# Kernel tuning notes

Measured on AMD Instinct MI355X. Metric: run time of the kernel, lower is better.

## Reference

```python
import jax, jax.numpy as jnp
import numpy as np
from jax import lax

BN_EPS = 1e-5
DIST_EPS = 1e-8

def _three_nn_interpolate(xyz1, xyz2, points2):
    # squared pairwise distances: (B, N, S)
    d2 = (jnp.sum(xyz1 ** 2, -1)[:, :, None]
          + jnp.sum(xyz2 ** 2, -1)[:, None, :]
          - 2.0 * jnp.einsum('bnd,bsd->bns', xyz1, xyz2))
    neg_d, idx = lax.top_k(-d2, 3)            # 3 nearest -> (B, N, 3)
    dist = -neg_d
    recip = 1.0 / (dist + DIST_EPS)
    weight = recip / jnp.sum(recip, -1, keepdims=True)   # (B, N, 3)
    gathered = jax.vmap(lambda p, i: p[i])(points2, idx)  # (B, N, 3, C2)
    return jnp.einsum('bnkc,bnk->bnc', gathered, weight)

def _conv_bn_relu(x, w, g, b):
    # x: (B, N, Cin); 1x1 conv == matmul; BatchNorm1d over (B, N) per channel (training stats)
    y = jnp.einsum('bnc,oc->bno', x, w)
    mu = jnp.mean(y, axis=(0, 1))
    var = jnp.mean((y - mu) ** 2, axis=(0, 1))
    yn = (y - mu) * lax.rsqrt(var + BN_EPS)
    return jax.nn.relu(yn * g + b)

def setup_inputs() -> dict:
    key = jax.random.key(0)
    ks = jax.random.split(key, 6)
    B, N, S, C1, C2 = 16, 4096, 1024, 256, 256
    return {
        'xyz1': jax.random.normal(ks[0], (B, N, 3), jnp.float32),
        'xyz2': jax.random.normal(ks[1], (B, S, 3), jnp.float32),
        'points1': jax.random.normal(ks[2], (B, N, C1), jnp.float32),
        'points2': jax.random.normal(ks[3], (B, S, C2), jnp.float32),
        'w1': jax.random.normal(ks[4], (256, C1 + C2), jnp.float32) * 0.04,
        'g1': jnp.ones((256,), jnp.float32),
        'b1': jnp.zeros((256,), jnp.float32),
        'w2': jax.random.normal(ks[5], (256, 256), jnp.float32) * 0.06,
        'g2': jnp.ones((256,), jnp.float32),
        'b2': jnp.zeros((256,), jnp.float32),
    }

def reference(xyz1, xyz2, points1, points2, w1, g1, b1, w2, g2, b2):
    interp = _three_nn_interpolate(xyz1, xyz2, points2)    # (B, N, C2)
    feats = jnp.concatenate([points1, interp], axis=-1)    # (B, N, C1+C2)
    h = _conv_bn_relu(feats, w1, g1, b1)
    out = _conv_bn_relu(h, w2, g2, b2)
    return out                                              # (B, N, 256)
```

## Files before the change

### kernel.cpp

```cpp
#include <hip/hip_runtime.h>
#include <stdint.h>

typedef unsigned short ushort_t;
typedef __bf16 bf16x8 __attribute__((ext_vector_type(8)));
typedef float f32x4 __attribute__((ext_vector_type(4)));
typedef unsigned short ushort8 __attribute__((ext_vector_type(8)));
typedef __attribute__((address_space(1))) void GVoid;
typedef __attribute__((address_space(3))) void LVoid;

#define DEV static __device__ __forceinline__

DEV unsigned short f2bf(float f) {
    union { float f; unsigned int i; } v; v.f = f;
    unsigned int u = v.i;
    return (unsigned short)((u + 0x7fffu + ((u >> 16) & 1u)) >> 16);
}
DEV float bf2f(unsigned short u) {
    union { unsigned int i; float f; } v; v.i = ((unsigned int)u) << 16; return v.f;
}

__global__ __launch_bounds__(256) void cvt_kernel(
    const float* __restrict__ in, ushort_t* __restrict__ out, int n)
{
    int i = blockIdx.x * 256 + threadIdx.x;
    if (i < n) out[i] = f2bf(in[i]);
}

__global__ __launch_bounds__(256) void knn_kernel(
    const float* __restrict__ xyz1, const float* __restrict__ xyz2,
    int* __restrict__ idx_out, float* __restrict__ w_out)
{
    __shared__ float4 P[1024];
    __shared__ float mD[12][64];
    __shared__ int   mI[12][64];
    const int b = blockIdx.y;
    const int tid = threadIdx.x;
    for (int s = tid; s < 1024; s += 256) {
        const float* p = xyz2 + ((size_t)b * 1024 + s) * 3;
        float x = p[0], y = p[1], z = p[2];
        float pp = __fadd_rn(__fadd_rn(__fmul_rn(x, x), __fmul_rn(y, y)), __fmul_rn(z, z));
        P[s] = make_float4(x, y, z, pp);
    }
    __syncthreads();
    const int ql = tid & 63;
    const int chunk = tid >> 6;
    const int n = blockIdx.x * 64 + ql;
    const float* q = xyz1 + ((size_t)b * 4096 + n) * 3;
    float qx = q[0], qy = q[1], qz = q[2];
    float qq = __fadd_rn(__fadd_rn(__fmul_rn(qx, qx), __fmul_rn(qy, qy)), __fmul_rn(qz, qz));
    float d0 = 1e30f, d1 = 1e30f, d2 = 1e30f;
    int i0 = 0, i1 = 0, i2 = 0;
    const int s0 = chunk * 256;
#pragma unroll 4
    for (int s = s0; s < s0 + 256; ++s) {
        float4 p = P[s];
        float dot = __fadd_rn(__fadd_rn(__fmul_rn(qx, p.x), __fmul_rn(qy, p.y)), __fmul_rn(qz, p.z));
        float d = __fsub_rn(__fadd_rn(qq, p.w), __fmul_rn(2.0f, dot));
        if (d < d2) {
            if (d < d1) {
                d2 = d1; i2 = i1;
                if (d < d0) { d1 = d0; i1 = i0; d0 = d; i0 = s; }
                else        { d1 = d;  i1 = s; }
            } else { d2 = d; i2 = s; }
        }
    }
    mD[chunk * 3 + 0][ql] = d0; mI[chunk * 3 + 0][ql] = i0;
    mD[chunk * 3 + 1][ql] = d1; mI[chunk * 3 + 1][ql] = i1;
    mD[chunk * 3 + 2][ql] = d2; mI[chunk * 3 + 2][ql] = i2;
    __syncthreads();
    if (tid < 64) {
        float e0 = 1e30f, e1 = 1e30f, e2 = 1e30f;
        int j0 = 0, j1 = 0, j2 = 0;
#pragma unroll
        for (int c = 0; c < 12; ++c) {
            float d = mD[c][ql]; int i = mI[c][ql];
            if (d < e2) {
                if (d < e1) {
                    e2 = e1; j2 = j1;
                    if (d < e0) { e1 = e0; j1 = j0; e0 = d; j0 = i; }
                    else        { e1 = d;  j1 = i; }
                } else { e2 = d; j2 = i; }
            }
        }
        float r0 = 1.0f / (e0 + 1e-8f);
        float r1 = 1.0f / (e1 + 1e-8f);
        float r2 = 1.0f / (e2 + 1e-8f);
        float rs = __fadd_rn(__fadd_rn(r0, r1), r2);
        size_t o = ((size_t)b * 4096 + n) * 3;
        idx_out[o + 0] = j0; idx_out[o + 1] = j1; idx_out[o + 2] = j2;
        w_out[o + 0] = r0 / rs; w_out[o + 1] = r1 / rs; w_out[o + 2] = r2 / rs;
    }
}

__global__ __launch_bounds__(256) void gemm1_kernel(
    const float* __restrict__ p1, const float* __restrict__ points2,
    const int* __restrict__ idx, const float* __restrict__ wgt,
    const ushort_t* __restrict__ w1b, ushort_t* __restrict__ y)
{
    __shared__ ushort_t As[64 * 32];
    __shared__ ushort_t Bs[256 * 32];
    __shared__ int   sIdx[192];
    __shared__ float sWgt[192];
    const int tid = threadIdx.x;
    const int wave = tid >> 6, lane = tid & 63;
    const int fr = lane & 15, fq = lane >> 4;
    const int m0 = blockIdx.x * 64;
    const int sr = tid >> 2, sq = tid & 3;

    if (tid < 192) { sIdx[tid] = idx[(size_t)m0 * 3 + tid]; sWgt[tid] = wgt[(size_t)m0 * 3 + tid]; }

    const float* p2base = points2 + (size_t)(m0 >> 12) * (1024 * 256);

    f32x4 acc[4][4];
#pragma unroll
    for (int i = 0; i < 4; ++i)
#pragma unroll
        for (int j = 0; j < 4; ++j) acc[i][j] = f32x4{0.0f, 0.0f, 0.0f, 0.0f};

    for (int kc = 0; kc < 16; ++kc) {
        __syncthreads();
#pragma unroll
        for (int p = 0; p < 4; ++p) {
            const ushort_t* g = w1b + (size_t)(p * 64 + sr) * 512 + kc * 32 + sq * 8;
            __builtin_amdgcn_global_load_lds((GVoid*)g, (LVoid*)(Bs + p * 2048 + wave * 512), 16, 0, 0);
        }
        {
            const int r = sr;
            const int c0 = sq * 8;
            float v[8];
            if (kc < 8) {
                const float4* g = (const float4*)(p1 + (size_t)(m0 + r) * 256 + kc * 32 + c0);
                float4 u0 = g[0], u1 = g[1];
                v[0] = u0.x; v[1] = u0.y; v[2] = u0.z; v[3] = u0.w;
                v[4] = u1.x; v[5] = u1.y; v[6] = u1.z; v[7] = u1.w;
            } else {
                const int ka = (kc - 8) * 32 + c0;
                int i0 = sIdx[r * 3 + 0], i1 = sIdx[r * 3 + 1], i2 = sIdx[r * 3 + 2];
                float w0 = sWgt[r * 3 + 0], w1 = sWgt[r * 3 + 1], w2 = sWgt[r * 3 + 2];
                const float4* g0 = (const float4*)(p2base + (size_t)i0 * 256 + ka);
                const float4* g1 = (const float4*)(p2base + (size_t)i1 * 256 + ka);
                const float4* g2 = (const float4*)(p2base + (size_t)i2 * 256 + ka);
                float4 a0 = g0[0], a1 = g0[1];
                float4 b0 = g1[0], b1 = g1[1];
                float4 c0v = g2[0], c1v = g2[1];
                v[0] = fmaf(w2, c0v.x, fmaf(w1, b0.x, __fmul_rn(w0, a0.x)));
                v[1] = fmaf(w2, c0v.y, fmaf(w1, b0.y, __fmul_rn(w0, a0.y)));
                v[2] = fmaf(w2, c0v.z, fmaf(w1, b0.z, __fmul_rn(w0, a0.z)));
                v[3] = fmaf(w2, c0v.w, fmaf(w1, b0.w, __fmul_rn(w0, a0.w)));
                v[4] = fmaf(w2, c1v.x, fmaf(w1, b1.x, __fmul_rn(w0, a1.x)));
                v[5] = fmaf(w2, c1v.y, fmaf(w1, b1.y, __fmul_rn(w0, a1.y)));
                v[6] = fmaf(w2, c1v.z, fmaf(w1, b1.z, __fmul_rn(w0, a1.z)));
                v[7] = fmaf(w2, c1v.w, fmaf(w1, b1.w, __fmul_rn(w0, a1.w)));
            }
            ushort8 hv;
#pragma unroll
            for (int j = 0; j < 8; ++j) hv[j] = f2bf(v[j]);
            *(ushort8*)(As + tid * 8) = hv;
        }
        __syncthreads();
        bf16x8 af[4], bfr[4];
#pragma unroll
        for (int i = 0; i < 4; ++i)
            af[i] = *(const bf16x8*)(As + (i * 16 + fr) * 32 + fq * 8);
#pragma unroll
        for (int j = 0; j < 4; ++j)
            bfr[j] = *(const bf16x8*)(Bs + (wave * 64 + j * 16 + fr) * 32 + fq * 8);
#pragma unroll
        for (int i = 0; i < 4; ++i)
#pragma unroll
            for (int j = 0; j < 4; ++j)
                acc[i][j] = __builtin_amdgcn_mfma_f32_16x16x32_bf16(af[i], bfr[j], acc[i][j], 0, 0, 0);
    }
#pragma unroll
    for (int i = 0; i < 4; ++i)
#pragma unroll
        for (int j = 0; j < 4; ++j)
#pragma unroll
            for (int r = 0; r < 4; ++r) {
                int row = m0 + i * 16 + fq * 4 + r;
                int col = wave * 64 + j * 16 + fr;
                y[(size_t)row * 256 + col] = f2bf(acc[i][j][r]);
            }
}

__global__ __launch_bounds__(256) void gemm2_kernel(
    const ushort_t* __restrict__ y1, const ushort_t* __restrict__ w2b,
    const float* __restrict__ a1, const float* __restrict__ c1,
    float* __restrict__ y2)
{
    __shared__ ushort_t As[64 * 32];
    __shared__ ushort_t Bs[256 * 32];
    __shared__ float sA[256], sC[256];
    const int tid = threadIdx.x;
    sA[tid] = a1[tid]; sC[tid] = c1[tid];
    const int wave = tid >> 6, lane = tid & 63;
    const int fr = lane & 15, fq = lane >> 4;
    const int m0 = blockIdx.x * 64;
    const int sr = tid >> 2, sq = tid & 3;

    f32x4 acc[4][4];
#pragma unroll
    for (int i = 0; i < 4; ++i)
#pragma unroll
        for (int j = 0; j < 4; ++j) acc[i][j] = f32x4{0.0f, 0.0f, 0.0f, 0.0f};

    for (int kc = 0; kc < 8; ++kc) {
        const int k0 = kc * 32;
        __syncthreads();
#pragma unroll
        for (int p = 0; p < 4; ++p) {
            const ushort_t* g = w2b + (size_t)(p * 64 + sr) * 256 + k0 + sq * 8;
            __builtin_amdgcn_global_load_lds((GVoid*)g, (LVoid*)(Bs + p * 2048 + wave * 512), 16, 0, 0);
        }
        {
            ushort8 raw = *(const ushort8*)(y1 + (size_t)(m0 + sr) * 256 + k0 + sq * 8);
            ushort8 hv;
#pragma unroll
            for (int j = 0; j < 8; ++j) {
                int ch = k0 + sq * 8 + j;
                float v = bf2f(raw[j]);
                hv[j] = f2bf(fmaxf(fmaf(v, sA[ch], sC[ch]), 0.0f));
            }
            *(ushort8*)(As + tid * 8) = hv;
        }
        __syncthreads();
        bf16x8 af[4], bfr[4];
#pragma unroll
        for (int i = 0; i < 4; ++i)
            af[i] = *(const bf16x8*)(As + (i * 16 + fr) * 32 + fq * 8);
#pragma unroll
        for (int j = 0; j < 4; ++j)
            bfr[j] = *(const bf16x8*)(Bs + (wave * 64 + j * 16 + fr) * 32 + fq * 8);
#pragma unroll
        for (int i = 0; i < 4; ++i)
#pragma unroll
            for (int j = 0; j < 4; ++j)
                acc[i][j] = __builtin_amdgcn_mfma_f32_16x16x32_bf16(af[i], bfr[j], acc[i][j], 0, 0, 0);
    }
#pragma unroll
    for (int i = 0; i < 4; ++i)
#pragma unroll
        for (int j = 0; j < 4; ++j)
#pragma unroll
            for (int r = 0; r < 4; ++r) {
                int row = m0 + i * 16 + fq * 4 + r;
                int col = wave * 64 + j * 16 + fr;
                y2[(size_t)row * 256 + col] = acc[i][j][r];
            }
}

__global__ __launch_bounds__(256) void stats_bf16_kernel(
    const ushort_t* __restrict__ y, float* __restrict__ sums, float* __restrict__ sqs)
{
    const int c = threadIdx.x;
    const size_t r0 = (size_t)blockIdx.x * 128;
    float s0 = 0, s1 = 0, q0 = 0, q1 = 0;
    for (int r = 0; r < 128; r += 2) {
        float v0 = bf2f(y[(r0 + r + 0) * 256 + c]);
        float v1 = bf2f(y[(r0 + r + 1) * 256 + c]);
        s0 += v0; q0 = fmaf(v0, v0, q0);
        s1 += v1; q1 = fmaf(v1, v1, q1);
    }
    atomicAdd(&sums[c], s0 + s1);
    atomicAdd(&sqs[c], q0 + q1);
}

__global__ __launch_bounds__(256) void stats_f32_kernel(
    const float* __restrict__ y, float* __restrict__ sums, float* __restrict__ sqs)
{
    const int c = threadIdx.x;
    const size_t r0 = (size_t)blockIdx.x * 128;
    float s0 = 0, s1 = 0, q0 = 0, q1 = 0;
    for (int r = 0; r < 128; r += 2) {
        float v0 = y[(r0 + r + 0) * 256 + c];
        float v1 = y[(r0 + r + 1) * 256 + c];
        s0 += v0; q0 = fmaf(v0, v0, q0);
        s1 += v1; q1 = fmaf(v1, v1, q1);
    }
    atomicAdd(&sums[c], s0 + s1);
    atomicAdd(&sqs[c], q0 + q1);
}

__global__ __launch_bounds__(256) void finalize_kernel(
    const float* __restrict__ sums, const float* __restrict__ sqs,
    const float* __restrict__ g, const float* __restrict__ bias,
    float* __restrict__ a, float* __restrict__ c)
{
    const int ch = threadIdx.x;
    const float inv_n = 1.0f / 65536.0f;
    float mu = sums[ch] * inv_n;
    float var = fmaf(-mu, mu, sqs[ch] * inv_n);
    float is = 1.0f / sqrtf(var + 1e-5f);
    float aa = g[ch] * is;
    a[ch] = aa;
    c[ch] = fmaf(-mu, aa, bias[ch]);
}

__global__ __launch_bounds__(256) void apply_kernel(
    float* __restrict__ y2, const float* __restrict__ a, const float* __restrict__ c)
{
    const size_t i = ((size_t)blockIdx.x * 256 + threadIdx.x) * 4;
    const int ch = (int)(i & 255);
    float4 v = *(const float4*)(y2 + i);
    const float4 av = *(const float4*)(a + ch);
    const float4 cv = *(const float4*)(c + ch);
    v.x = fmaxf(fmaf(v.x, av.x, cv.x), 0.0f);
    v.y = fmaxf(fmaf(v.y, av.y, cv.y), 0.0f);
    v.z = fmaxf(fmaf(v.z, av.z, cv.z), 0.0f);
    v.w = fmaxf(fmaf(v.w, av.w, cv.w), 0.0f);
    *(float4*)(y2 + i) = v;
}

extern "C" void kernel_launch(void* const* d_in, const int* in_sizes, int n_in,
                              void* d_out, int out_size, void* d_ws, size_t ws_size,
                              hipStream_t stream)
{
    const float* xyz1    = (const float*)d_in[0];
    const float* xyz2    = (const float*)d_in[1];
    const float* points1 = (const float*)d_in[2];
    const float* points2 = (const float*)d_in[3];
    const float* w1      = (const float*)d_in[4];
    const float* g1      = (const float*)d_in[5];
    const float* b1      = (const float*)d_in[6];
    const float* w2      = (const float*)d_in[7];
    const float* g2      = (const float*)d_in[8];
    const float* b2      = (const float*)d_in[9];
    float* out = (float*)d_out;

    char* ws = (char*)d_ws;
    float* sums1 = (float*)(ws + 0);
    float* sqs1  = (float*)(ws + 1024);
    float* a1    = (float*)(ws + 2048);
    float* c1    = (float*)(ws + 3072);
    float* sums2 = (float*)(ws + 4096);
    float* sqs2  = (float*)(ws + 5120);
    float* a2    = (float*)(ws + 6144);
    float* c2    = (float*)(ws + 7168);
    ushort_t* w1b = (ushort_t*)(ws + (64u << 10));
    ushort_t* w2b = (ushort_t*)(ws + (320u << 10));
    int*   idx   = (int*)(ws + (1u << 20));
    float* wgt   = (float*)(ws + (2u << 20));
    ushort_t* y1 = (ushort_t*)(ws + (4u << 20));

    hipMemsetAsync(ws, 0, 8192, stream);
    cvt_kernel<<<dim3(512), 256, 0, stream>>>(w1, w1b, 131072);
    cvt_kernel<<<dim3(256), 256, 0, stream>>>(w2, w2b, 65536);
    knn_kernel<<<dim3(64, 16), 256, 0, stream>>>(xyz1, xyz2, idx, wgt);
    gemm1_kernel<<<dim3(1024), 256, 0, stream>>>(points1, points2, idx, wgt, w1b, y1);
    stats_bf16_kernel<<<dim3(512), 256, 0, stream>>>(y1, sums1, sqs1);
    finalize_kernel<<<dim3(1), 256, 0, stream>>>(sums1, sqs1, g1, b1, a1, c1);
    gemm2_kernel<<<dim3(1024), 256, 0, stream>>>(y1, w2b, a1, c1, out);
    stats_f32_kernel<<<dim3(512), 256, 0, stream>>>(out, sums2, sqs2);
    finalize_kernel<<<dim3(1), 256, 0, stream>>>(sums2, sqs2, g2, b2, a2, c2);
    apply_kernel<<<dim3(16384), 256, 0, stream>>>(out, a2, c2);
}
```

Baseline: 302.9 us.

## Fuse BN stats into GEMM epilogues and stage full A tile in LDS

Both GEMM kernels now stage the whole 64-row A tile (all K) in LDS once, with an XOR swizzle for gemm1 and padding for gemm2. Weight fragments are read straight from global memory into registers with double buffering, so the per-K-step barriers and LDS B staging go away. The per-channel sum and sum-of-squares are computed in the GEMM epilogues with wave shuffles and atomics, which removes the two separate stats kernels and their re-reads of y1 and out. The cost is a larger LDS footprint (64 KB in gemm1), which may lower occupancy, and uncached-style global B loads for every wave.

New measurement: 309.7 us. +2.2%, slower.

```diff
diff --git a/kernel.cpp b/kernel.cpp
--- a/kernel.cpp
+++ b/kernel.cpp
@@ -5,8 +5,6 @@
 typedef __bf16 bf16x8 __attribute__((ext_vector_type(8)));
 typedef float f32x4 __attribute__((ext_vector_type(4)));
 typedef unsigned short ushort8 __attribute__((ext_vector_type(8)));
-typedef __attribute__((address_space(1))) void GVoid;
-typedef __attribute__((address_space(3))) void LVoid;
 
 #define DEV static __device__ __forceinline__
 
@@ -92,24 +90,63 @@
     }
 }
 
+DEV void cvt8(const float4& u0, const float4& u1, ushort8& hv) {
+    hv[0] = f2bf(u0.x); hv[1] = f2bf(u0.y); hv[2] = f2bf(u0.z); hv[3] = f2bf(u0.w);
+    hv[4] = f2bf(u1.x); hv[5] = f2bf(u1.y); hv[6] = f2bf(u1.z); hv[7] = f2bf(u1.w);
+}
+
 __global__ __launch_bounds__(256) void gemm1_kernel(
     const float* __restrict__ p1, const float* __restrict__ points2,
     const int* __restrict__ idx, const float* __restrict__ wgt,
-    const ushort_t* __restrict__ w1b, ushort_t* __restrict__ y)
-{
-    __shared__ ushort_t As[64 * 32];
-    __shared__ ushort_t Bs[256 * 32];
-    __shared__ int   sIdx[192];
-    __shared__ float sWgt[192];
+    const ushort_t* __restrict__ w1b, ushort_t* __restrict__ y,
+    float* __restrict__ sums, float* __restrict__ sqs)
+{
+    __shared__ ushort_t As[64 * 512];
     const int tid = threadIdx.x;
     const int wave = tid >> 6, lane = tid & 63;
-    const int fr = lane & 15, fq = lane >> 4;
+    const int frl = lane & 15, fq = lane >> 4;
+    const int fr7 = frl & 7;
     const int m0 = blockIdx.x * 64;
-    const int sr = tid >> 2, sq = tid & 3;
-
-    if (tid < 192) { sIdx[tid] = idx[(size_t)m0 * 3 + tid]; sWgt[tid] = wgt[(size_t)m0 * 3 + tid]; }
-
-    const float* p2base = points2 + (size_t)(m0 >> 12) * (1024 * 256);
+
+    {
+        const int r = tid >> 2, cg = tid & 3;
+        ushort_t* dst = As + r * 512;
+        const float4* gp = (const float4*)(p1 + (size_t)(m0 + r) * 256 + cg * 64);
+#pragma unroll
+        for (int jj = 0; jj < 8; ++jj) {
+            float4 u0 = gp[2 * jj], u1 = gp[2 * jj + 1];
+            ushort8 hv; cvt8(u0, u1, hv);
+            int cb = cg * 8 + jj;
+            *(ushort8*)(dst + ((cb ^ (r & 7)) << 3)) = hv;
+        }
+        const size_t qo = (size_t)(m0 + r) * 3;
+        int i0 = idx[qo], i1 = idx[qo + 1], i2 = idx[qo + 2];
+        float w0 = wgt[qo], w1 = wgt[qo + 1], w2 = wgt[qo + 2];
+        const float* pb = points2 + (size_t)(m0 >> 12) * (1024 * 256);
+        const float4* g0 = (const float4*)(pb + (size_t)i0 * 256 + cg * 64);
+        const float4* g1 = (const float4*)(pb + (size_t)i1 * 256 + cg * 64);
+        const float4* g2 = (const float4*)(pb + (size_t)i2 * 256 + cg * 64);
+#pragma unroll
+        for (int jj = 0; jj < 8; ++jj) {
+            float4 a0 = g0[2 * jj], a1 = g0[2 * jj + 1];
+            float4 b0 = g1[2 * jj], b1 = g1[2 * jj + 1];
+            float4 c0 = g2[2 * jj], c1 = g2[2 * jj + 1];
+            float v[8];
+            v[0] = fmaf(w2, c0.x, fmaf(w1, b0.x, __fmul_rn(w0, a0.x)));
+            v[1] = fmaf(w2, c0.y, fmaf(w1, b0.y, __fmul_rn(w0, a0.y)));
+            v[2] = fmaf(w2, c0.z, fmaf(w1, b0.z, __fmul_rn(w0, a0.z)));
+            v[3] = fmaf(w2, c0.w, fmaf(w1, b0.w, __fmul_rn(w0, a0.w)));
+            v[4] = fmaf(w2, c1.x, fmaf(w1, b1.x, __fmul_rn(w0, a1.x)));
+            v[5] = fmaf(w2, c1.y, fmaf(w1, b1.y, __fmul_rn(w0, a1.y)));
+            v[6] = fmaf(w2, c1.z, fmaf(w1, b1.z, __fmul_rn(w0, a1.z)));
+            v[7] = fmaf(w2, c1.w, fmaf(w1, b1.w, __fmul_rn(w0, a1.w)));
+            ushort8 hv;
+#pragma unroll
+            for (int j = 0; j < 8; ++j) hv[j] = f2bf(v[j]);
+            int cb = 32 + cg * 8 + jj;
+            *(ushort8*)(dst + ((cb ^ (r & 7)) << 3)) = hv;
+        }
+    }
 
     f32x4 acc[4][4];
 #pragma unroll
@@ -117,168 +154,122 @@
 #pragma unroll
         for (int j = 0; j < 4; ++j) acc[i][j] = f32x4{0.0f, 0.0f, 0.0f, 0.0f};
 
-    for (int kc = 0; kc < 16; ++kc) {
-        __syncthreads();
-#pragma unroll
-        for (int p = 0; p < 4; ++p) {
-            const ushort_t* g = w1b + (size_t)(p * 64 + sr) * 512 + kc * 32 + sq * 8;
-            __builtin_amdgcn_global_load_lds((GVoid*)g, (LVoid*)(Bs + p * 2048 + wave * 512), 16, 0, 0);
-        }
-        {
-            const int r = sr;
-            const int c0 = sq * 8;
-            float v[8];
-            if (kc < 8) {
-                const float4* g = (const float4*)(p1 + (size_t)(m0 + r) * 256 + kc * 32 + c0);
-                float4 u0 = g[0], u1 = g[1];
-                v[0] = u0.x; v[1] = u0.y; v[2] = u0.z; v[3] = u0.w;
-                v[4] = u1.x; v[5] = u1.y; v[6] = u1.z; v[7] = u1.w;
-            } else {
-                const int ka = (kc - 8) * 32 + c0;
-                int i0 = sIdx[r * 3 + 0], i1 = sIdx[r * 3 + 1], i2 = sIdx[r * 3 + 2];
-                float w0 = sWgt[r * 3 + 0], w1 = sWgt[r * 3 + 1], w2 = sWgt[r * 3 + 2];
-                const float4* g0 = (const float4*)(p2base + (size_t)i0 * 256 + ka);
-                const float4* g1 = (const float4*)(p2base + (size_t)i1 * 256 + ka);
-                const float4* g2 = (const float4*)(p2base + (size_t)i2 * 256 + ka);
-                float4 a0 = g0[0], a1 = g0[1];
-                float4 b0 = g1[0], b1 = g1[1];
-                float4 c0v = g2[0], c1v = g2[1];
-                v[0] = fmaf(w2, c0v.x, fmaf(w1, b0.x, __fmul_rn(w0, a0.x)));
-                v[1] = fmaf(w2, c0v.y, fmaf(w1, b0.y, __fmul_rn(w0, a0.y)));
-                v[2] = fmaf(w2, c0v.z, fmaf(w1, b0.z, __fmul_rn(w0, a0.z)));
-                v[3] = fmaf(w2, c0v.w, fmaf(w1, b0.w, __fmul_rn(w0, a0.w)));
-                v[4] = fmaf(w2, c1v.x, fmaf(w1, b1.x, __fmul_rn(w0, a1.x)));
-                v[5] = fmaf(w2, c1v.y, fmaf(w1, b1.y, __fmul_rn(w0, a1.y)));
-                v[6] = fmaf(w2, c1v.z, fmaf(w1, b1.z, __fmul_rn(w0, a1.z)));
-                v[7] = fmaf(w2, c1v.w, fmaf(w1, b1.w, __fmul_rn(w0, a1.w)));
+    __syncthreads();
+
+    const ushort_t* wb = w1b + (size_t)(wave * 64 + frl) * 512 + fq * 8;
+    bf16x8 aA[4], aB[4], bA[4], bB[4];
+
+#define LOADB1(dst, kc) { _Pragma("unroll") \
+    for (int j = 0; j < 4; ++j) dst[j] = *(const bf16x8*)(wb + j * (16 * 512) + (kc) * 32); }
+#define LOADA1(dst, kc) { _Pragma("unroll") \
+    for (int i = 0; i < 4; ++i) dst[i] = *(const bf16x8*)(As + (i * 16 + frl) * 512 + (((((kc) << 2) + fq) ^ fr7) << 3)); }
+#define MF16(a, b) { _Pragma("unroll") \
+    for (int i = 0; i < 4; ++i) { _Pragma("unroll") \
+        for (int j = 0; j < 4; ++j) \
+            acc[i][j] = __builtin_amdgcn_mfma_f32_16x16x32_bf16(a[i], b[j], acc[i][j], 0, 0, 0); } }
+
+    LOADA1(aA, 0); LOADB1(bA, 0);
+#pragma unroll
+    for (int kc = 0; kc < 16; kc += 2) {
+        LOADA1(aB, kc + 1); LOADB1(bB, kc + 1);
+        MF16(aA, bA);
+        if (kc + 2 < 16) { LOADA1(aA, kc + 2); LOADB1(bA, kc + 2); }
+        MF16(aB, bB);
+    }
+
+#pragma unroll
+    for (int j = 0; j < 4; ++j) {
+        const int col = wave * 64 + j * 16 + frl;
+        float s = 0.f, q = 0.f;
+#pragma unroll
+        for (int i = 0; i < 4; ++i)
+#pragma unroll
+            for (int rr = 0; rr < 4; ++rr) {
+                ushort_t hb = f2bf(acc[i][j][rr]);
+                float v = bf2f(hb);
+                y[(size_t)(m0 + i * 16 + fq * 4 + rr) * 256 + col] = hb;
+                s += v; q = fmaf(v, v, q);
             }
-            ushort8 hv;
-#pragma unroll
-            for (int j = 0; j < 8; ++j) hv[j] = f2bf(v[j]);
-            *(ushort8*)(As + tid * 8) = hv;
-        }
-        __syncthreads();
-        bf16x8 af[4], bfr[4];
-#pragma unroll
-        for (int i = 0; i < 4; ++i)
-            af[i] = *(const bf16x8*)(As + (i * 16 + fr) * 32 + fq * 8);
-#pragma unroll
-        for (int j = 0; j < 4; ++j)
-            bfr[j] = *(const bf16x8*)(Bs + (wave * 64 + j * 16 + fr) * 32 + fq * 8);
-#pragma unroll
-        for (int i = 0; i < 4; ++i)
-#pragma unroll
-            for (int j = 0; j < 4; ++j)
-                acc[i][j] = __builtin_amdgcn_mfma_f32_16x16x32_bf16(af[i], bfr[j], acc[i][j], 0, 0, 0);
-    }
-#pragma unroll
-    for (int i = 0; i < 4; ++i)
-#pragma unroll
-        for (int j = 0; j < 4; ++j)
-#pragma unroll
-            for (int r = 0; r < 4; ++r) {
-                int row = m0 + i * 16 + fq * 4 + r;
-                int col = wave * 64 + j * 16 + fr;
-                y[(size_t)row * 256 + col] = f2bf(acc[i][j][r]);
-            }
+        s += __shfl_xor(s, 16); s += __shfl_xor(s, 32);
+        q += __shfl_xor(q, 16); q += __shfl_xor(q, 32);
+        if (fq == 0) { atomicAdd(&sums[col], s); atomicAdd(&sqs[col], q); }
+    }
 }
 
 __global__ __launch_bounds__(256) void gemm2_kernel(
     const ushort_t* __restrict__ y1, const ushort_t* __restrict__ w2b,
     const float* __restrict__ a1, const float* __restrict__ c1,
-    float* __restrict__ y2)
-{
-    __shared__ ushort_t As[64 * 32];
-    __shared__ ushort_t Bs[256 * 32];
+    float* __restrict__ y2, float* __restrict__ sums, float* __restrict__ sqs)
+{
+    __shared__ ushort_t As[64 * 264];
     __shared__ float sA[256], sC[256];
     const int tid = threadIdx.x;
+    const int wave = tid >> 6, lane = tid & 63;
+    const int frl = lane & 15, fq = lane >> 4;
+    const int m0 = blockIdx.x * 64;
+
     sA[tid] = a1[tid]; sC[tid] = c1[tid];
-    const int wave = tid >> 6, lane = tid & 63;
-    const int fr = lane & 15, fq = lane >> 4;
-    const int m0 = blockIdx.x * 64;
-    const int sr = tid >> 2, sq = tid & 3;
-
-    f32x4 acc[4][4];
-#pragma unroll
-    for (int i = 0; i < 4; ++i)
-#pragma unroll
-        for (int j = 0; j < 4; ++j) acc[i][j] = f32x4{0.0f, 0.0f, 0.0f, 0.0f};
-
-    for (int kc = 0; kc < 8; ++kc) {
-        const int k0 = kc * 32;
-        __syncthreads();
-#pragma unroll
-        for (int p = 0; p < 4; ++p) {
-            const ushort_t* g = w2b + (size_t)(p * 64 + sr) * 256 + k0 + sq * 8;
-            __builtin_amdgcn_global_load_lds((GVoid*)g, (LVoid*)(Bs + p * 2048 + wave * 512), 16, 0, 0);
-        }
-        {
-            ushort8 raw = *(const ushort8*)(y1 + (size_t)(m0 + sr) * 256 + k0 + sq * 8);
+    __syncthreads();
+
+    {
+        const int r = tid >> 2, cg = tid & 3;
+        const ushort8* gp = (const ushort8*)(y1 + (size_t)(m0 + r) * 256 + cg * 64);
+        ushort_t* dst = As + r * 264 + cg * 64;
+#pragma unroll
+        for (int jj = 0; jj < 8; ++jj) {
+            ushort8 raw = gp[jj];
             ushort8 hv;
 #pragma unroll
             for (int j = 0; j < 8; ++j) {
-                int ch = k0 + sq * 8 + j;
+                int ch = cg * 64 + jj * 8 + j;
                 float v = bf2f(raw[j]);
                 hv[j] = f2bf(fmaxf(fmaf(v, sA[ch], sC[ch]), 0.0f));
             }
-            *(ushort8*)(As + tid * 8) = hv;
-        }
-        __syncthreads();
-        bf16x8 af[4], bfr[4];
+            *(ushort8*)(dst + jj * 8) = hv;
+        }
+    }
+
+    f32x4 acc[4][4];
+#pragma unroll
+    for (int i = 0; i < 4; ++i)
+#pragma unroll
+        for (int j = 0; j < 4; ++j) acc[i][j] = f32x4{0.0f, 0.0f, 0.0f, 0.0f};
+
+    __syncthreads();
+
+    const ushort_t* wb = w2b + (size_t)(wave * 64 + frl) * 256 + fq * 8;
+    bf16x8 aA[4], aB[4], bA[4], bB[4];
+
+#define LOADB2(dst, kc) { _Pragma("unroll") \
+    for (int j = 0; j < 4; ++j) dst[j] = *(const bf16x8*)(wb + j * (16 * 256) + (kc) * 32); }
+#define LOADA2(dst, kc) { _Pragma("unroll") \
+    for (int i = 0; i < 4; ++i) dst[i] = *(const bf16x8*)(As + (i * 16 + frl) * 264 + (kc) * 32 + fq * 8); }
+
+    LOADA2(aA, 0); LOADB2(bA, 0);
+#pragma unroll
+    for (int kc = 0; kc < 8; kc += 2) {
+        LOADA2(aB, kc + 1); LOADB2(bB, kc + 1);
+        MF16(aA, bA);
+        if (kc + 2 < 8) { LOADA2(aA, kc + 2); LOADB2(bA, kc + 2); }
+        MF16(aB, bB);
+    }
+
+#pragma unroll
+    for (int j = 0; j < 4; ++j) {
+        const int col = wave * 64 + j * 16 + frl;
+        float s = 0.f, q = 0.f;
 #pragma unroll
         for (int i = 0; i < 4; ++i)
-            af[i] = *(const bf16x8*)(As + (i * 16 + fr) * 32 + fq * 8);
-#pragma unroll
-        for (int j = 0; j < 4; ++j)
-            bfr[j] = *(const bf16x8*)(Bs + (wave * 64 + j * 16 + fr) * 32 + fq * 8);
-#pragma unroll
-        for (int i = 0; i < 4; ++i)
-#pragma unroll
-            for (int j = 0; j < 4; ++j)
-                acc[i][j] = __builtin_amdgcn_mfma_f32_16x16x32_bf16(af[i], bfr[j], acc[i][j], 0, 0, 0);
-    }
-#pragma unroll
-    for (int i = 0; i < 4; ++i)
-#pragma unroll
-        for (int j = 0; j < 4; ++j)
-#pragma unroll
-            for (int r = 0; r < 4; ++r) {
-                int row = m0 + i * 16 + fq * 4 + r;
-                int col = wave * 64 + j * 16 + fr;
-                y2[(size_t)row * 256 + col] = acc[i][j][r];
+#pragma unroll
+            for (int rr = 0; rr < 4; ++rr) {
+                float v = acc[i][j][rr];
+                y2[(size_t)(m0 + i * 16 + fq * 4 + rr) * 256 + col] = v;
+                s += v; q = fmaf(v, v, q);
             }
-}
-
-__global__ __launch_bounds__(256) void stats_bf16_kernel(
-    const ushort_t* __restrict__ y, float* __restrict__ sums, float* __restrict__ sqs)
-{
-    const int c = threadIdx.x;
-    const size_t r0 = (size_t)blockIdx.x * 128;
-    float s0 = 0, s1 = 0, q0 = 0, q1 = 0;
-    for (int r = 0; r < 128; r += 2) {
-        float v0 = bf2f(y[(r0 + r + 0) * 256 + c]);
-        float v1 = bf2f(y[(r0 + r + 1) * 256 + c]);
-        s0 += v0; q0 = fmaf(v0, v0, q0);
-        s1 += v1; q1 = fmaf(v1, v1, q1);
-    }
-    atomicAdd(&sums[c], s0 + s1);
-    atomicAdd(&sqs[c], q0 + q1);
-}
-
-__global__ __launch_bounds__(256) void stats_f32_kernel(
-    const float* __restrict__ y, float* __restrict__ sums, float* __restrict__ sqs)
-{
-    const int c = threadIdx.x;
-    const size_t r0 = (size_t)blockIdx.x * 128;
-    float s0 = 0, s1 = 0, q0 = 0, q1 = 0;
-    for (int r = 0; r < 128; r += 2) {
-        float v0 = y[(r0 + r + 0) * 256 + c];
-        float v1 = y[(r0 + r + 1) * 256 + c];
-        s0 += v0; q0 = fmaf(v0, v0, q0);
-        s1 += v1; q1 = fmaf(v1, v1, q1);
-    }
-    atomicAdd(&sums[c], s0 + s1);
-    atomicAdd(&sqs[c], q0 + q1);
+        s += __shfl_xor(s, 16); s += __shfl_xor(s, 32);
+        q += __shfl_xor(q, 16); q += __shfl_xor(q, 32);
+        if (fq == 0) { atomicAdd(&sums[col], s); atomicAdd(&sqs[col], q); }
+    }
 }
 
 __global__ __launch_bounds__(256) void finalize_kernel(
@@ -346,11 +337,9 @@
     cvt_kernel<<<dim3(512), 256, 0, stream>>>(w1, w1b, 131072);
     cvt_kernel<<<dim3(256), 256, 0, stream>>>(w2, w2b, 65536);
     knn_kernel<<<dim3(64, 16), 256, 0, stream>>>(xyz1, xyz2, idx, wgt);
-    gemm1_kernel<<<dim3(1024), 256, 0, stream>>>(points1, points2, idx, wgt, w1b, y1);
-    stats_bf16_kernel<<<dim3(512), 256, 0, stream>>>(y1, sums1, sqs1);
+    gemm1_kernel<<<dim3(1024), 256, 0, stream>>>(points1, points2, idx, wgt, w1b, y1, sums1, sqs1);
     finalize_kernel<<<dim3(1), 256, 0, stream>>>(sums1, sqs1, g1, b1, a1, c1);
-    gemm2_kernel<<<dim3(1024), 256, 0, stream>>>(y1, w2b, a1, c1, out);
-    stats_f32_kernel<<<dim3(512), 256, 0, stream>>>(out, sums2, sqs2);
+    gemm2_kernel<<<dim3(1024), 256, 0, stream>>>(y1, w2b, a1, c1, out, sums2, sqs2);
     finalize_kernel<<<dim3(1), 256, 0, stream>>>(sums2, sqs2, g2, b2, a2, c2);
     apply_kernel<<<dim3(16384), 256, 0, stream>>>(out, a2, c2);
 }
```
